# Optimization experiments

Hardware: AMD Instinct MI355X
Metric: run time of the kernel (lower is better)

## Reference

```python
import jax, jax.numpy as jnp
import numpy as np

M1, M2, M3 = 16, 16, 3  # Fourier mode truncation (modes3 hard-coded to 3 in torch __init__)


def setup_inputs() -> dict:
    key = jax.random.key(0)
    k0, k1, k2, k3, k4 = jax.random.split(key, 5)
    B, Ci, Co, T, X, P = 8, 32, 32, 128, 256, 3
    scale = 1.0 / (Ci * Co)
    x = jax.random.normal(k0, (B, Ci, T, X, P), dtype=jnp.float32)
    w1_re = scale * jax.random.uniform(k1, (Ci, Co, M1, M2, M3), dtype=jnp.float32)
    w1_im = scale * jax.random.uniform(k2, (Ci, Co, M1, M2, M3), dtype=jnp.float32)
    w2_re = scale * jax.random.uniform(k3, (Ci, Co, M1, M2, M3), dtype=jnp.float32)
    w2_im = scale * jax.random.uniform(k4, (Ci, Co, M1, M2, M3), dtype=jnp.float32)
    return {"x": x, "w1_re": w1_re, "w1_im": w1_im, "w2_re": w2_re, "w2_im": w2_im}


def reference(x, w1_re, w1_im, w2_re, w2_im):
    # x: [B, Ci, T, X, P] -- pipes pre-stacked along last dim (method == 34 branch)
    B, Ci, T, X, P = x.shape
    Co = w1_re.shape[1]
    w1 = (w1_re + 1j * w1_im).astype(jnp.complex64)
    w2 = (w2_re + 1j * w2_im).astype(jnp.complex64)

    x_ft = jnp.fft.rfftn(x, axes=(2, 3, 4))          # [B, Ci, T, X, P//2+1]
    z = min(x_ft.shape[4], M3)                       # torch: z_dim = min(x_ft.shape[4], modes3)

    # low-x / low-y corner
    coeff1 = jnp.zeros((B, Ci, M1, M2, M3), jnp.complex64)
    coeff1 = coeff1.at[..., :z].set(x_ft[:, :, :M1, :M2, :z])
    blk1 = jnp.einsum('bixyz,ioxyz->boxyz', coeff1, w1)

    # high-x / low-y corner
    coeff2 = jnp.zeros((B, Ci, M1, M2, M3), jnp.complex64)
    coeff2 = coeff2.at[..., :z].set(x_ft[:, :, -M1:, :M2, :z])
    blk2 = jnp.einsum('bixyz,ioxyz->boxyz', coeff2, w2)

    out_ft = jnp.zeros((B, Co, T, X, P), jnp.complex64)
    out_ft = out_ft.at[:, :, :M1, :M2, :M3].set(blk1)
    out_ft = out_ft.at[:, :, -M1:, :M2, :M3].set(blk2)

    # irfftn with s=(T, X, P) crops last axis to P//2+1 coeffs, matching torch semantics
    out = jnp.fft.irfftn(out_ft, s=(T, X, P), axes=(-3, -2, -1))  # [B, Co, T, X, P] float32
    return out
```

## Files before the change

### kernel.cpp

```cpp
#include <hip/hip_runtime.h>
#include <math.h>

typedef float2 F2;

__device__ __forceinline__ F2 cmul(F2 a, F2 b) {
    return make_float2(a.x * b.x - a.y * b.y, a.x * b.y + a.y * b.x);
}
__device__ __forceinline__ F2 cmac(F2 acc, F2 a, F2 b) {
    acc.x += a.x * b.x - a.y * b.y;
    acc.y += a.x * b.y + a.y * b.x;
    return acc;
}

#define TWO_PI 6.283185307179586f
#define SQRT3_2 0.8660254037844386f
#define SQRT3 1.7320508075688772f

__global__ __launch_bounds__(256) void k1_fwd_x(const float* __restrict__ x,
                                                F2* __restrict__ y) {
    __shared__ float xp0[8][260];
    __shared__ F2    xp1[8][260];
    __shared__ F2    tw[256];
    __shared__ F2    part[1024];
    const int tid = threadIdx.x;
    const int blk = blockIdx.x;

    {
        float sv, cv;
        sincosf(-TWO_PI * (float)tid * (1.0f / 256.0f), &sv, &cv);
        tw[tid] = make_float2(cv, sv);
    }
#pragma unroll
    for (int j = 0; j < 8; ++j) {
        int item = tid + 256 * j;
        int row = item >> 8, xx = item & 255;
        const float* src = x + ((size_t)(blk * 8 + row) * 256 + xx) * 3;
        float a = src[0], b = src[1], c = src[2];
        xp0[row][xx] = a + b + c;
        xp1[row][xx] = make_float2(a - 0.5f * (b + c), SQRT3_2 * (c - b));
    }
    __syncthreads();

    const int kz = tid >> 7, rr = (tid >> 4) & 7, kxg = (tid >> 2) & 3, c = tid & 3;
    const float sgn = (kxg & 1) ? -1.0f : 1.0f;

    F2 acc[4], w[4], stp[4];
#pragma unroll
    for (int u = 0; u < 4; ++u) {
        int kx = kxg + 4 * u;
        acc[u] = make_float2(0.f, 0.f);
        w[u] = tw[(kx * c) & 255];
        stp[u] = tw[(4 * kx) & 255];
    }

    if (kz == 0) {
        const float* r0 = xp0[rr];
#pragma unroll 8
        for (int m = 0; m < 32; ++m) {
            int xx = c + 4 * m;
            float s = fmaf(sgn, r0[xx + 128], r0[xx]);
#pragma unroll
            for (int u = 0; u < 4; ++u) {
                acc[u].x = fmaf(s, w[u].x, acc[u].x);
                acc[u].y = fmaf(s, w[u].y, acc[u].y);
                w[u] = cmul(w[u], stp[u]);
            }
        }
    } else {
        const F2* r1 = xp1[rr];
#pragma unroll 8
        for (int m = 0; m < 32; ++m) {
            int xx = c + 4 * m;
            F2 a = r1[xx], b = r1[xx + 128];
            F2 s = make_float2(fmaf(sgn, b.x, a.x), fmaf(sgn, b.y, a.y));
#pragma unroll
            for (int u = 0; u < 4; ++u) {
                acc[u] = cmac(acc[u], s, w[u]);
                w[u] = cmul(w[u], stp[u]);
            }
        }
    }

#pragma unroll
    for (int u = 0; u < 4; ++u) {
        int kx = kxg + 4 * u;
        part[(((rr * 2 + kz) * 16 + kx) << 2) + c] = acc[u];
    }
    __syncthreads();
    {
        int rr2 = tid >> 5, kz2 = (tid >> 4) & 1, kx2 = tid & 15;
        const F2* p = &part[((rr2 * 2 + kz2) * 16 + kx2) << 2];
        F2 r = p[0];
        r.x += p[1].x + p[2].x + p[3].x;
        r.y += p[1].y + p[2].y + p[3].y;
        y[((size_t)(blk * 8 + rr2) * 2 + kz2) * 16 + kx2] = r;
    }
}

__global__ __launch_bounds__(256) void k2a_fwd_t(const F2* __restrict__ y,
                                                 F2* __restrict__ xft) {
    __shared__ F2 yL[128][16];
    const int tid = threadIdx.x;
    const int bi = blockIdx.x >> 1, kz = blockIdx.x & 1;
#pragma unroll
    for (int j = 0; j < 8; ++j) {
        int item = tid + 256 * j;
        int t = item >> 4, kx = item & 15;
        yL[t][kx] = y[((size_t)(bi * 128 + t) * 2 + kz) * 16 + kx];
    }
    __syncthreads();

    const int kx = tid & 15, sg = tid >> 4;
    F2 rotA = make_float2(1.f, 0.f), rotB = make_float2(1.f, 0.f), stepA, stepB;
    sincosf(-TWO_PI * (float)sg * (1.0f / 128.0f), &stepA.y, &stepA.x);
    sincosf(-TWO_PI * (float)(112 + sg) * (1.0f / 128.0f), &stepB.y, &stepB.x);
    F2 accA = make_float2(0.f, 0.f), accB = make_float2(0.f, 0.f);
#pragma unroll 8
    for (int t = 0; t < 128; ++t) {
        F2 v = yL[t][kx];
        accA = cmac(accA, v, rotA);
        accB = cmac(accB, v, rotB);
        rotA = cmul(rotA, stepA);
        rotB = cmul(rotB, stepB);
    }
    const int b = bi >> 5, i = bi & 31;
    xft[(((size_t)(b * 32 + sg) * 2 + kz) * 16 + kx) * 32 + i] = accA;
    xft[(((size_t)(b * 32 + (16 + sg)) * 2 + kz) * 16 + kx) * 32 + i] = accB;
}

__global__ __launch_bounds__(256) void k2b_mix(const F2* __restrict__ xft,
                                               const float* __restrict__ w1re,
                                               const float* __restrict__ w1im,
                                               const float* __restrict__ w2re,
                                               const float* __restrict__ w2im,
                                               F2* __restrict__ blkout) {
    __shared__ F2 xL[512];
    __shared__ F2 wcL[2][32][32];
    const int tid = threadIdx.x;
    const int s = blockIdx.x >> 4, kx = blockIdx.x & 15;
#pragma unroll
    for (int j = 0; j < 2; ++j) {
        int item = tid + 256 * j;
        int b = item >> 6, kz = (item >> 5) & 1, i = item & 31;
        xL[item] = xft[(((size_t)(b * 32 + s) * 2 + kz) * 16 + kx) * 32 + i];
    }
    const float* bre = (s < 16) ? w1re : w2re;
    const float* bim = (s < 16) ? w1im : w2im;
    const int m1 = s & 15;
#pragma unroll
    for (int j = 0; j < 4; ++j) {
        int iop = tid + 256 * j;
        int i = iop >> 5, o = iop & 31;
        size_t g = (((size_t)(i * 32 + o) * 16 + m1) * 16 + kx) * 3;
        wcL[0][i][o] = make_float2(bre[g], bim[g]);
        wcL[1][i][o] = make_float2(bre[g + 1], bim[g + 1]);
    }
    __syncthreads();

    const int b = tid >> 5, o = tid & 31;
#pragma unroll
    for (int kz = 0; kz < 2; ++kz) {
        F2 acc = make_float2(0.f, 0.f);
#pragma unroll 8
        for (int i = 0; i < 32; ++i) {
            F2 xv = xL[(b * 2 + kz) * 32 + i];
            F2 wv = wcL[kz][i][o];
            acc.x += xv.x * wv.x - xv.y * wv.y;
            acc.y += xv.x * wv.y + xv.y * wv.x;
        }
        blkout[(((size_t)(b * 32 + o) * 32 + s) * 2 + kz) * 16 + kx] = acc;
    }
}

__global__ __launch_bounds__(256) void k2c_inv_t(const F2* __restrict__ blkin,
                                                 F2* __restrict__ h) {
    __shared__ F2 bL[1024];
    const int tid = threadIdx.x;
    const int bo = blockIdx.x >> 2, tc = blockIdx.x & 3;
#pragma unroll
    for (int j = 0; j < 4; ++j) {
        int item = tid + 256 * j;
        bL[item] = blkin[(size_t)bo * 1024 + item];
    }
    __syncthreads();

    const int col = tid & 31, tl = tid >> 5;
    F2 accA[4], accB[4], w[4], stp[4];
#pragma unroll
    for (int q = 0; q < 4; ++q) {
        accA[q] = make_float2(0.f, 0.f);
        accB[q] = make_float2(0.f, 0.f);
        w[q] = make_float2(1.f, 0.f);
        int t = 32 * tc + tl + 8 * q;
        sincosf(TWO_PI * (float)t * (1.0f / 128.0f), &stp[q].y, &stp[q].x);
    }
#pragma unroll 4
    for (int sp = 0; sp < 16; ++sp) {
        F2 bA = bL[sp * 32 + col];
        F2 bB = bL[(16 + sp) * 32 + col];
#pragma unroll
        for (int q = 0; q < 4; ++q) {
            accA[q] = cmac(accA[q], bA, w[q]);
            accB[q] = cmac(accB[q], bB, w[q]);
            w[q] = cmul(w[q], stp[q]);
        }
    }
    F2 phase;
    sincosf(-TWO_PI * (float)tl * (1.0f / 8.0f), &phase.y, &phase.x);
#pragma unroll
    for (int q = 0; q < 4; ++q) {
        int t = 32 * tc + tl + 8 * q;
        F2 r = cmac(accA[q], phase, accB[q]);
        h[((size_t)bo * 128 + t) * 32 + col] = r;
    }
}

__global__ __launch_bounds__(256) void k3_inv_x(const F2* __restrict__ h,
                                                float* __restrict__ out) {
    __shared__ F2 hL[64];
    __shared__ float oL[1536];
    const int tid = threadIdx.x;
    const int blk = blockIdx.x;
    if (tid < 64) hL[tid] = h[(size_t)blk * 64 + tid];
    __syncthreads();

    const int rr = tid >> 7, x = tid & 127;
    const F2* hrow = &hL[rr * 32];
    F2 w = make_float2(1.f, 0.f), r;
    sincosf(TWO_PI * (float)x * (1.0f / 256.0f), &r.y, &r.x);
    float e0 = 0.f, o0 = 0.f;
    F2 e1 = make_float2(0.f, 0.f), o1 = make_float2(0.f, 0.f);
#pragma unroll
    for (int k2 = 0; k2 < 8; ++k2) {
        {
            F2 h0 = hrow[2 * k2], h1 = hrow[16 + 2 * k2];
            e0 += h0.x * w.x - h0.y * w.y;
            e1.x += h1.x * w.x - h1.y * w.y;
            e1.y += h1.x * w.y + h1.y * w.x;
            w = cmul(w, r);
        }
        {
            F2 h0 = hrow[2 * k2 + 1], h1 = hrow[16 + 2 * k2 + 1];
            o0 += h0.x * w.x - h0.y * w.y;
            o1.x += h1.x * w.x - h1.y * w.y;
            o1.y += h1.x * w.y + h1.y * w.x;
            w = cmul(w, r);
        }
    }
    const float n = 1.0f / 98304.0f;
    float* o = &oL[rr * 768];
    {
        float g0 = e0 + o0, g1r = e1.x + o1.x, g1i = e1.y + o1.y;
        o[x * 3 + 0] = n * (g0 + 2.f * g1r);
        o[x * 3 + 1] = n * (g0 - g1r - SQRT3 * g1i);
        o[x * 3 + 2] = n * (g0 - g1r + SQRT3 * g1i);
    }
    {
        float g0 = e0 - o0, g1r = e1.x - o1.x, g1i = e1.y - o1.y;
        int xb = x + 128;
        o[xb * 3 + 0] = n * (g0 + 2.f * g1r);
        o[xb * 3 + 1] = n * (g0 - g1r - SQRT3 * g1i);
        o[xb * 3 + 2] = n * (g0 - g1r + SQRT3 * g1i);
    }
    __syncthreads();
    {
        float4* dst = (float4*)(out + (size_t)blk * 1536);
        const float4* src = (const float4*)oL;
        dst[tid] = src[tid];
        if (tid < 128) dst[tid + 256] = src[tid + 256];
    }
}

extern "C" void kernel_launch(void* const* d_in, const int* in_sizes, int n_in,
                              void* d_out, int out_size, void* d_ws, size_t ws_size,
                              hipStream_t stream) {
    const float* x    = (const float*)d_in[0];
    const float* w1re = (const float*)d_in[1];
    const float* w1im = (const float*)d_in[2];
    const float* w2re = (const float*)d_in[3];
    const float* w2im = (const float*)d_in[4];
    float* out = (float*)d_out;

    F2* y   = (F2*)d_ws;
    F2* xft = y + 1048576;
    F2* bk  = xft + 262144;
    F2* h   = bk + 262144;

    hipLaunchKernelGGL(k1_fwd_x,  dim3(4096),  dim3(256), 0, stream, x, y);
    hipLaunchKernelGGL(k2a_fwd_t, dim3(512),   dim3(256), 0, stream, y, xft);
    hipLaunchKernelGGL(k2b_mix,   dim3(512),   dim3(256), 0, stream, xft,
                       w1re, w1im, w2re, w2im, bk);
    hipLaunchKernelGGL(k2c_inv_t, dim3(1024),  dim3(256), 0, stream, bk, h);
    hipLaunchKernelGGL(k3_inv_x,  dim3(16384), dim3(256), 0, stream, h, out);
}
```

Measured before the change: 260.5 us.

## Factor x-axis truncated DFT in k1 into radix-4 butterflies with constant twiddles

Replaces the direct 32-step DFT accumulation per thread (with a recurrence-updated twiddle per output mode) with a factored scheme. Four strided inputs are first combined into two partial sums using per-kxg twiddles, then an 8-step loop applies compile-time twiddles from constant tables and final per-c post-twiddles. This cuts the number of complex multiplies and twiddle recurrences in the forward x-transform. In exchange it uses more registers (T0/T1 arrays) and more LDS reads per step.

```diff
diff --git a/kernel.cpp b/kernel.cpp
--- a/kernel.cpp
+++ b/kernel.cpp
@@ -15,6 +15,15 @@
 #define TWO_PI 6.283185307179586f
 #define SQRT3_2 0.8660254037844386f
 #define SQRT3 1.7320508075688772f
+
+__device__ constexpr float TW16X[16] = {
+    1.f,  0.923879533f,  0.707106781f,  0.382683432f,  0.f, -0.382683432f,
+    -0.707106781f, -0.923879533f, -1.f, -0.923879533f, -0.707106781f,
+    -0.382683432f, 0.f,  0.382683432f,  0.707106781f,  0.923879533f};
+__device__ constexpr float TW16Y[16] = {
+    0.f, -0.382683432f, -0.707106781f, -0.923879533f, -1.f, -0.923879533f,
+    -0.707106781f, -0.382683432f, 0.f,  0.382683432f,  0.707106781f,
+    0.923879533f,  1.f,  0.923879533f,  0.707106781f,  0.382683432f};
 
 __global__ __launch_bounds__(256) void k1_fwd_x(const float* __restrict__ x,
                                                 F2* __restrict__ y) {
@@ -44,47 +53,83 @@
     const int kz = tid >> 7, rr = (tid >> 4) & 7, kxg = (tid >> 2) & 3, c = tid & 3;
     const float sgn = (kxg & 1) ? -1.0f : 1.0f;
 
-    F2 acc[4], w[4], stp[4];
-#pragma unroll
-    for (int u = 0; u < 4; ++u) {
-        int kx = kxg + 4 * u;
-        acc[u] = make_float2(0.f, 0.f);
-        w[u] = tw[(kx * c) & 255];
-        stp[u] = tw[(4 * kx) & 255];
-    }
-
+    const F2 c01 = tw[(32 * kxg) & 255];
+    const F2 c02 = tw[(64 * kxg) & 255];
+    const F2 c03 = tw[(96 * kxg) & 255];
+    const F2 f1 = tw[(4 * c) & 255];
+    const F2 f2 = tw[(8 * c) & 255];
+    const F2 f3 = tw[(12 * c) & 255];
+
+    F2 T0[8], T1[8];
     if (kz == 0) {
         const float* r0 = xp0[rr];
-#pragma unroll 8
-        for (int m = 0; m < 32; ++m) {
-            int xx = c + 4 * m;
-            float s = fmaf(sgn, r0[xx + 128], r0[xx]);
-#pragma unroll
-            for (int u = 0; u < 4; ++u) {
-                acc[u].x = fmaf(s, w[u].x, acc[u].x);
-                acc[u].y = fmaf(s, w[u].y, acc[u].y);
-                w[u] = cmul(w[u], stp[u]);
-            }
+#pragma unroll
+        for (int b = 0; b < 8; ++b) {
+            int x0 = c + 4 * b;
+            float s0 = fmaf(sgn, r0[x0 + 128], r0[x0]);
+            float s1 = fmaf(sgn, r0[x0 + 160], r0[x0 + 32]);
+            float s2 = fmaf(sgn, r0[x0 + 192], r0[x0 + 64]);
+            float s3 = fmaf(sgn, r0[x0 + 224], r0[x0 + 96]);
+            F2 p1 = make_float2(s1 * c01.x, s1 * c01.y);
+            F2 p2 = make_float2(s2 * c02.x, s2 * c02.y);
+            F2 p3 = make_float2(s3 * c03.x, s3 * c03.y);
+            T0[b] = make_float2(s0 + p1.x + p2.x + p3.x, p1.y + p2.y + p3.y);
+            T1[b] = make_float2(s0 - p1.x + p2.x - p3.x, -p1.y + p2.y - p3.y);
         }
     } else {
         const F2* r1 = xp1[rr];
-#pragma unroll 8
-        for (int m = 0; m < 32; ++m) {
-            int xx = c + 4 * m;
-            F2 a = r1[xx], b = r1[xx + 128];
-            F2 s = make_float2(fmaf(sgn, b.x, a.x), fmaf(sgn, b.y, a.y));
-#pragma unroll
-            for (int u = 0; u < 4; ++u) {
-                acc[u] = cmac(acc[u], s, w[u]);
-                w[u] = cmul(w[u], stp[u]);
-            }
-        }
-    }
-
-#pragma unroll
-    for (int u = 0; u < 4; ++u) {
-        int kx = kxg + 4 * u;
-        part[(((rr * 2 + kz) * 16 + kx) << 2) + c] = acc[u];
+#pragma unroll
+        for (int b = 0; b < 8; ++b) {
+            int x0 = c + 4 * b;
+            F2 a0 = r1[x0],      b0 = r1[x0 + 128];
+            F2 a1 = r1[x0 + 32], b1 = r1[x0 + 160];
+            F2 a2 = r1[x0 + 64], b2 = r1[x0 + 192];
+            F2 a3 = r1[x0 + 96], b3 = r1[x0 + 224];
+            F2 s0 = make_float2(fmaf(sgn, b0.x, a0.x), fmaf(sgn, b0.y, a0.y));
+            F2 s1 = make_float2(fmaf(sgn, b1.x, a1.x), fmaf(sgn, b1.y, a1.y));
+            F2 s2 = make_float2(fmaf(sgn, b2.x, a2.x), fmaf(sgn, b2.y, a2.y));
+            F2 s3 = make_float2(fmaf(sgn, b3.x, a3.x), fmaf(sgn, b3.y, a3.y));
+            F2 p1 = cmul(s1, c01);
+            F2 p2 = cmul(s2, c02);
+            F2 p3 = cmul(s3, c03);
+            T0[b] = make_float2(s0.x + p1.x + p2.x + p3.x, s0.y + p1.y + p2.y + p3.y);
+            T1[b] = make_float2(s0.x - p1.x + p2.x - p3.x, s0.y - p1.y + p2.y - p3.y);
+        }
+    }
+
+    F2 acc0 = make_float2(0.f, 0.f), acc1 = acc0, acc2 = acc0, acc3 = acc0;
+#pragma unroll
+    for (int b = 0; b < 8; ++b) {
+        F2 tb = tw[(kxg * (c + 4 * b)) & 255];
+        F2 q0 = cmul(tb, T0[b]);
+        F2 q1 = cmul(tb, T1[b]);
+        acc0.x += q0.x; acc0.y += q0.y;
+        {
+            const float Cx = TW16X[(2 * b) & 15], Cy = TW16Y[(2 * b) & 15];
+            acc2.x += q0.x * Cx - q0.y * Cy;
+            acc2.y += q0.x * Cy + q0.y * Cx;
+        }
+        {
+            const float Cx = TW16X[b & 15], Cy = TW16Y[b & 15];
+            acc1.x += q1.x * Cx - q1.y * Cy;
+            acc1.y += q1.x * Cy + q1.y * Cx;
+        }
+        {
+            const float Cx = TW16X[(3 * b) & 15], Cy = TW16Y[(3 * b) & 15];
+            acc3.x += q1.x * Cx - q1.y * Cy;
+            acc3.y += q1.x * Cy + q1.y * Cx;
+        }
+    }
+    acc1 = cmul(acc1, f1);
+    acc2 = cmul(acc2, f2);
+    acc3 = cmul(acc3, f3);
+
+    {
+        const int base = (((rr * 2 + kz) * 16 + kxg) << 2) + c;
+        part[base]       = acc0;
+        part[base + 16]  = acc1;
+        part[base + 32]  = acc2;
+        part[base + 48]  = acc3;
     }
     __syncthreads();
     {
```

Measured after the change: 253.7 us. -2.6%, faster.
